# Kernel tuning notes

Hardware: AMD Instinct MI355X
Metric: run time of the kernel (lower is better)

## Reference

```python
import jax, jax.numpy as jnp
import numpy as np

RTOL = 1e-3
ATOL = 1e-3
MAX_STEPS = 16   # static bound on adaptive dopri5 iterations (accepted+rejected)
H0 = 0.05        # initial step size (torchdiffeq picks this heuristically)


def _mlp(t1, y, z, w1, b1, w2, b2, t_eval):
    # TimeRescale: t = t1 * t_eval; dH/dt1 = hazard(t, y, z) * t_eval
    tt = t1 * t_eval                                   # [B,1]
    x = jnp.concatenate([tt, y, z], axis=1)            # [B, latent+2]
    h = jax.nn.relu(x @ w1.T + b1)                     # [B, 2*(latent+2)]
    return jax.nn.softplus(h @ w2.T + b2) * t_eval     # [B,1]


def _dopri5(f, y0, t1=1.0):
    """Adaptive Dormand-Prince RK45 from t=0 to t=t1 with a static step budget."""
    f0 = f(jnp.float32(0.0), y0)

    def body(i, carry):
        t, y, fy, h, done = carry
        h = jnp.minimum(h, t1 - t)
        k1 = fy
        k2 = f(t + 0.2 * h, y + h * (0.2 * k1))
        k3 = f(t + 0.3 * h, y + h * (3/40 * k1 + 9/40 * k2))
        k4 = f(t + 0.8 * h, y + h * (44/45 * k1 - 56/15 * k2 + 32/9 * k3))
        k5 = f(t + 8/9 * h, y + h * (19372/6561 * k1 - 25360/2187 * k2 + 64448/6561 * k3 - 212/729 * k4))
        k6 = f(t + h, y + h * (9017/3168 * k1 - 355/33 * k2 + 46732/5247 * k3 + 49/176 * k4 - 5103/18656 * k5))
        y5 = y + h * (35/384 * k1 + 500/1113 * k3 + 125/192 * k4 - 2187/6784 * k5 + 11/84 * k6)
        k7 = f(t + h, y5)  # FSAL
        err = h * (71/57600 * k1 - 71/16695 * k3 + 71/1920 * k4 - 17253/339200 * k5 + 22/525 * k6 - 1/40 * k7)
        scale = ATOL + RTOL * jnp.maximum(jnp.abs(y), jnp.abs(y5))
        en = jnp.sqrt(jnp.mean((err / scale) ** 2))
        accept = (en <= 1.0) & (~done)
        fac = jnp.clip(0.9 * jnp.power(jnp.maximum(en, 1e-10), -0.2), 0.2, 10.0)
        t_n = jnp.where(accept, t + h, t)
        y_n = jnp.where(accept, y5, y)
        f_n = jnp.where(accept, k7, fy)
        h_n = jnp.where(done, h, h * fac)
        done_n = done | (t_n >= t1 - 1e-9)
        return (t_n, y_n, f_n, h_n, done_n)

    carry = (jnp.float32(0.0), y0, f0, jnp.float32(H0), jnp.array(False))
    _, yT, _, _, _ = jax.lax.fori_loop(0, MAX_STEPS, body, carry)
    return yT


def setup_inputs() -> dict:
    key = jax.random.key(0)
    ks = jax.random.split(key, 6)
    B, D, R = 4096, 128, 2
    IN, HID = D + 2, 2 * (D + 2)
    s = 1.0 / np.sqrt(IN)
    return {
        "z": jax.random.normal(ks[0], (B, D), jnp.float32),
        "t_eval": jax.random.uniform(ks[1], (B, 1), jnp.float32, 0.1, 3.0),
        "w1": jax.random.normal(ks[2], (R, HID, IN), jnp.float32) * s,
        "b1": jax.random.normal(ks[3], (R, HID), jnp.float32) * s,
        "w2": jax.random.normal(ks[4], (R, 1, HID), jnp.float32) * (1.0 / np.sqrt(HID)),
        "b2": jax.random.normal(ks[5], (R, 1), jnp.float32) * 0.01,
    }


def reference(z, t_eval, w1, b1, w2, b2):
    B = z.shape[0]
    R = w1.shape[0]
    y0 = jnp.zeros((B, 1), z.dtype)
    t_rec = jnp.where(t_eval != 0, 1.0 / t_eval, 0.0)
    haz_list, chf_list = [], []
    for r in range(R):
        f = lambda t, y, r=r: _mlp(t, y, z, w1[r], b1[r], w2[r], b2[r], t_eval)
        yT = _dopri5(f, y0)                       # CHF at rescaled t=1
        haz = t_rec * f(jnp.float32(1.0), yT)     # [B,1]
        chf = jnp.stack([y0, yT], axis=0)          # [2,B,1] (t_points = [0,1])
        chf_list.append(jnp.transpose(chf, (1, 0, 2)))  # [B,2,1]
        haz_list.append(haz.T)                           # [1,B]
    return (jnp.stack(haz_list, axis=0), jnp.stack(chf_list, axis=0))  # [R,1,B], [R,B,2,1]
```

## Files before the change

### kernel.cpp

```cpp
#include <hip/hip_runtime.h>
#include <math.h>


#define B_ 4096
#define R_ 2
#define D_ 128
#define IN_ 130
#define HID_ 260
#define NU_ 17
#define JP_ 272
#define KP_ 136

#define WS_P_      0
#define WS_ACW_    (R_ * B_ * JP_)

typedef __attribute__((ext_vector_type(8))) short  short8;
typedef __attribute__((ext_vector_type(4))) float  floatx4;

__device__ __forceinline__ unsigned short f2bf_rn(float x) {
    unsigned int u = __float_as_uint(x);
    unsigned int r = (u + 0x7FFFu + ((u >> 16) & 1u)) >> 16;
    return (unsigned short)r;
}
__device__ __forceinline__ float bf2f(unsigned short h) {
    return __uint_as_float(((unsigned int)h) << 16);
}

__global__ __launch_bounds__(256) void k1_gemm(
    const float* __restrict__ z, const float* __restrict__ w1,
    const float* __restrict__ b1, const float* __restrict__ w2,
    float* __restrict__ ws)
{
    __shared__ unsigned short sWh[64 * KP_];
    __shared__ unsigned short sWl[64 * KP_];
    __shared__ unsigned short sZh[64 * KP_];
    __shared__ unsigned short sZl[64 * KP_];

    const int t  = threadIdx.x;
    const int r  = blockIdx.x / 320;
    const int jt = (blockIdx.x % 320) >> 6;
    const int bt = blockIdx.x & 63;
    const int j0 = jt * 64;
    const int b0 = bt * 64;

    const float* w1r = w1 + r * HID_ * IN_;

    if (bt == 0 && t < 64) {
        const int j = j0 + t;
        if (j < HID_) {
            const float2 ac = *(const float2*)(w1r + j * IN_);
            float* acw = ws + WS_ACW_ + r * 3 * JP_;
            acw[0 * JP_ + j] = ac.x;
            acw[1 * JP_ + j] = ac.y;
            acw[2 * JP_ + j] = w2[r * HID_ + j];
        }
    }

    {
        const int row = t >> 2;
        const int ks  = (t & 3) * 32;
        const float* src = z + (b0 + row) * D_ + ks;
        unsigned short* dh = sZh + row * KP_ + ks;
        unsigned short* dl = sZl + row * KP_ + ks;
#pragma unroll
        for (int q = 0; q < 8; ++q) {
            const float4 v = *(const float4*)(src + q * 4);
            short4 hq, lq;
            {
                const unsigned short h0 = f2bf_rn(v.x); const float p0 = v.x - bf2f(h0);
                const unsigned short h1 = f2bf_rn(v.y); const float p1 = v.y - bf2f(h1);
                const unsigned short h2 = f2bf_rn(v.z); const float p2 = v.z - bf2f(h2);
                const unsigned short h3 = f2bf_rn(v.w); const float p3 = v.w - bf2f(h3);
                hq = make_short4((short)h0, (short)h1, (short)h2, (short)h3);
                lq = make_short4((short)f2bf_rn(p0), (short)f2bf_rn(p1),
                                 (short)f2bf_rn(p2), (short)f2bf_rn(p3));
            }
            *(short4*)(dh + q * 4) = hq;
            *(short4*)(dl + q * 4) = lq;
        }
    }

    {
        const int row = t >> 2;
        const int ks  = (t & 3) * 32;
        const int j   = j0 + row;
        unsigned short* dh = sWh + row * KP_ + ks;
        unsigned short* dl = sWl + row * KP_ + ks;
        if (j < HID_) {
            const float* src = w1r + j * IN_ + 2 + ks;
#pragma unroll
            for (int q = 0; q < 16; ++q) {
                const float2 v = *(const float2*)(src + q * 2);
                const unsigned short h0 = f2bf_rn(v.x); const float p0 = v.x - bf2f(h0);
                const unsigned short h1 = f2bf_rn(v.y); const float p1 = v.y - bf2f(h1);
                *(short2*)(dh + q * 2) = make_short2((short)h0, (short)h1);
                *(short2*)(dl + q * 2) = make_short2((short)f2bf_rn(p0), (short)f2bf_rn(p1));
            }
        } else {
            const short4 zz = make_short4(0, 0, 0, 0);
#pragma unroll
            for (int q = 0; q < 8; ++q) {
                *(short4*)(dh + q * 4) = zz;
                *(short4*)(dl + q * 4) = zz;
            }
        }
    }
    __syncthreads();

    const int wv   = t >> 6;
    const int lane = t & 63;
    const int lm   = lane & 15;
    const int quad = lane >> 4;

    short8 Ah[4], Al[4];
    {
        const unsigned short* aph = sWh + (wv * 16 + lm) * KP_ + quad * 8;
        const unsigned short* apl = sWl + (wv * 16 + lm) * KP_ + quad * 8;
#pragma unroll
        for (int ks = 0; ks < 4; ++ks) {
            Ah[ks] = *(const short8*)(aph + ks * 32);
            Al[ks] = *(const short8*)(apl + ks * 32);
        }
    }

    const int jrow = j0 + wv * 16 + quad * 4;
    float bj0 = 0.f, bj1 = 0.f, bj2 = 0.f, bj3 = 0.f;
    if (jrow < HID_) {
        const float* bb = b1 + r * HID_ + jrow;
        bj0 = bb[0]; bj1 = bb[1]; bj2 = bb[2]; bj3 = bb[3];
    }

#pragma unroll
    for (int bs = 0; bs < 4; ++bs) {
        floatx4 acc = {0.f, 0.f, 0.f, 0.f};
        const unsigned short* bph = sZh + (bs * 16 + lm) * KP_ + quad * 8;
        const unsigned short* bpl = sZl + (bs * 16 + lm) * KP_ + quad * 8;
#pragma unroll
        for (int ks = 0; ks < 4; ++ks) {
            const short8 Bh = *(const short8*)(bph + ks * 32);
            const short8 Bl = *(const short8*)(bpl + ks * 32);
            acc = __builtin_amdgcn_mfma_f32_16x16x32_bf16(Ah[ks], Bh, acc, 0, 0, 0);
            acc = __builtin_amdgcn_mfma_f32_16x16x32_bf16(Ah[ks], Bl, acc, 0, 0, 0);
            acc = __builtin_amdgcn_mfma_f32_16x16x32_bf16(Al[ks], Bh, acc, 0, 0, 0);
        }
        if (jrow < HID_) {
            const int b = b0 + bs * 16 + lm;
            float4 o;
            o.x = acc[0] + bj0;
            o.y = acc[1] + bj1;
            o.z = acc[2] + bj2;
            o.w = acc[3] + bj3;
            *(float4*)(ws + WS_P_ + (r * B_ + b) * JP_ + jrow) = o;
        }
    }
}

__device__ __forceinline__ float dpp_add16(float v) {
    int y;
    y = __builtin_amdgcn_update_dpp(0, __float_as_int(v), 0xB1, 0xF, 0xF, false);
    v += __int_as_float(y);
    y = __builtin_amdgcn_update_dpp(0, __float_as_int(v), 0x4E, 0xF, 0xF, false);
    v += __int_as_float(y);
    y = __builtin_amdgcn_update_dpp(0, __float_as_int(v), 0x124, 0xF, 0xF, false);
    v += __int_as_float(y);
    y = __builtin_amdgcn_update_dpp(0, __float_as_int(v), 0x128, 0xF, 0xF, false);
    v += __int_as_float(y);
    return v;
}

__device__ __forceinline__ float softplus_fast(float x) {
    const float q  = exp2f(-1.4426950408889634f * fabsf(x));
    const float lg = 0.6931471805599453f * log2f(1.0f + q);
    return fmaxf(x, 0.0f) + lg;
}

__global__ __launch_bounds__(256) void k2_solve(
    const float* __restrict__ t_eval, const float* __restrict__ b2,
    const float* __restrict__ ws, float* __restrict__ out)
{
    const int sub = threadIdx.x & 15;
    const int T   = blockIdx.x * 16 + (threadIdx.x >> 4);
    const int r   = T >> 12;
    const int b   = T & (B_ - 1);

    const float te = t_eval[b];

    float P[NU_], A[NU_], C[NU_], W[NU_];
    const float* pp  = ws + WS_P_ + (r * B_ + b) * JP_;
    const float* acw = ws + WS_ACW_ + r * 3 * JP_;
#pragma unroll
    for (int i = 0; i < NU_; ++i) {
        const int j = sub + (i << 4);
        if (j < HID_) {
            P[i] = pp[j];
            A[i] = acw[0 * JP_ + j];
            C[i] = acw[1 * JP_ + j];
            W[i] = acw[2 * JP_ + j];
        } else {
            P[i] = A[i] = C[i] = W[i] = 0.f;
        }
    }
    const float b2r = b2[r];

    auto feval = [&](float t1, float yv) -> float {
        const float tt = t1 * te;
        float d0 = 0.f, d1 = 0.f;
#pragma unroll
        for (int i = 0; i < NU_; ++i) {
            const float hv = fmaf(tt, A[i], fmaf(yv, C[i], P[i]));
            if (i & 1) d1 = fmaf(W[i], fmaxf(hv, 0.f), d1);
            else       d0 = fmaf(W[i], fmaxf(hv, 0.f), d0);
        }
        const float dot = dpp_add16(d0 + d1);
        return softplus_fast(dot + b2r) * te;
    };

    const float h  = 0.125f;
    const float hh = 0.0625f;
    float y = 0.f;
#pragma unroll 1
    for (int s = 0; s < 8; ++s) {
        const float t0 = (float)s * h;
        const float k1 = feval(t0,      y);
        const float k2 = feval(t0 + hh, fmaf(hh, k1, y));
        const float k3 = feval(t0 + hh, fmaf(hh, k2, y));
        const float k4 = feval(t0 + h,  fmaf(h,  k3, y));
        y = fmaf(h * (1.f / 6.f), k1 + 2.f * (k2 + k3) + k4, y);
    }

    const float yT = y;
    const float hazf = feval(1.0f, yT);
    const float t_rec = (te != 0.f) ? (1.f / te) : 0.f;

    if (sub == 0) {
        out[r * B_ + b] = t_rec * hazf;
        const int base = R_ * B_ + (r * B_ + b) * 2;
        out[base + 0] = 0.f;
        out[base + 1] = yT;
    }
}

extern "C" void kernel_launch(void* const* d_in, const int* in_sizes, int n_in,
                              void* d_out, int out_size, void* d_ws, size_t ws_size,
                              hipStream_t stream) {
    const float* z      = (const float*)d_in[0];
    const float* t_eval = (const float*)d_in[1];
    const float* w1     = (const float*)d_in[2];
    const float* b1     = (const float*)d_in[3];
    const float* w2     = (const float*)d_in[4];
    const float* b2     = (const float*)d_in[5];
    float* out = (float*)d_out;
    float* ws  = (float*)d_ws;

    hipLaunchKernelGGL(k1_gemm, dim3(640), dim3(256), 0, stream,
                       z, w1, b1, w2, ws);
    hipLaunchKernelGGL(k2_solve, dim3(512), dim3(256), 0, stream,
                       t_eval, b2, ws, out);
}
```

Before: 86.80 us.

## Fuse GEMM prologue and ODE solve into one kernel using shared memory

Merges the bf16-split MFMA projection kernel and the per-row dopri5 solve kernel into a single kernel. Each block computes the hidden pre-activations for its 16 rows directly into LDS, removing the global workspace round trip and the second launch. In exchange every block re-reads and re-converts the full w1 matrix for its head, and the larger LDS footprint may reduce occupancy during the solve phase.

```diff
diff --git a/kernel.cpp b/kernel.cpp
--- a/kernel.cpp
+++ b/kernel.cpp
@@ -8,11 +8,8 @@
 #define IN_ 130
 #define HID_ 260
 #define NU_ 17
-#define JP_ 272
 #define KP_ 136
-
-#define WS_P_      0
-#define WS_ACW_    (R_ * B_ * JP_)
+#define PP_ 272
 
 typedef __attribute__((ext_vector_type(8))) short  short8;
 typedef __attribute__((ext_vector_type(4))) float  floatx4;
@@ -26,135 +23,6 @@
     return __uint_as_float(((unsigned int)h) << 16);
 }
 
-__global__ __launch_bounds__(256) void k1_gemm(
-    const float* __restrict__ z, const float* __restrict__ w1,
-    const float* __restrict__ b1, const float* __restrict__ w2,
-    float* __restrict__ ws)
-{
-    __shared__ unsigned short sWh[64 * KP_];
-    __shared__ unsigned short sWl[64 * KP_];
-    __shared__ unsigned short sZh[64 * KP_];
-    __shared__ unsigned short sZl[64 * KP_];
-
-    const int t  = threadIdx.x;
-    const int r  = blockIdx.x / 320;
-    const int jt = (blockIdx.x % 320) >> 6;
-    const int bt = blockIdx.x & 63;
-    const int j0 = jt * 64;
-    const int b0 = bt * 64;
-
-    const float* w1r = w1 + r * HID_ * IN_;
-
-    if (bt == 0 && t < 64) {
-        const int j = j0 + t;
-        if (j < HID_) {
-            const float2 ac = *(const float2*)(w1r + j * IN_);
-            float* acw = ws + WS_ACW_ + r * 3 * JP_;
-            acw[0 * JP_ + j] = ac.x;
-            acw[1 * JP_ + j] = ac.y;
-            acw[2 * JP_ + j] = w2[r * HID_ + j];
-        }
-    }
-
-    {
-        const int row = t >> 2;
-        const int ks  = (t & 3) * 32;
-        const float* src = z + (b0 + row) * D_ + ks;
-        unsigned short* dh = sZh + row * KP_ + ks;
-        unsigned short* dl = sZl + row * KP_ + ks;
-#pragma unroll
-        for (int q = 0; q < 8; ++q) {
-            const float4 v = *(const float4*)(src + q * 4);
-            short4 hq, lq;
-            {
-                const unsigned short h0 = f2bf_rn(v.x); const float p0 = v.x - bf2f(h0);
-                const unsigned short h1 = f2bf_rn(v.y); const float p1 = v.y - bf2f(h1);
-                const unsigned short h2 = f2bf_rn(v.z); const float p2 = v.z - bf2f(h2);
-                const unsigned short h3 = f2bf_rn(v.w); const float p3 = v.w - bf2f(h3);
-                hq = make_short4((short)h0, (short)h1, (short)h2, (short)h3);
-                lq = make_short4((short)f2bf_rn(p0), (short)f2bf_rn(p1),
-                                 (short)f2bf_rn(p2), (short)f2bf_rn(p3));
-            }
-            *(short4*)(dh + q * 4) = hq;
-            *(short4*)(dl + q * 4) = lq;
-        }
-    }
-
-    {
-        const int row = t >> 2;
-        const int ks  = (t & 3) * 32;
-        const int j   = j0 + row;
-        unsigned short* dh = sWh + row * KP_ + ks;
-        unsigned short* dl = sWl + row * KP_ + ks;
-        if (j < HID_) {
-            const float* src = w1r + j * IN_ + 2 + ks;
-#pragma unroll
-            for (int q = 0; q < 16; ++q) {
-                const float2 v = *(const float2*)(src + q * 2);
-                const unsigned short h0 = f2bf_rn(v.x); const float p0 = v.x - bf2f(h0);
-                const unsigned short h1 = f2bf_rn(v.y); const float p1 = v.y - bf2f(h1);
-                *(short2*)(dh + q * 2) = make_short2((short)h0, (short)h1);
-                *(short2*)(dl + q * 2) = make_short2((short)f2bf_rn(p0), (short)f2bf_rn(p1));
-            }
-        } else {
-            const short4 zz = make_short4(0, 0, 0, 0);
-#pragma unroll
-            for (int q = 0; q < 8; ++q) {
-                *(short4*)(dh + q * 4) = zz;
-                *(short4*)(dl + q * 4) = zz;
-            }
-        }
-    }
-    __syncthreads();
-
-    const int wv   = t >> 6;
-    const int lane = t & 63;
-    const int lm   = lane & 15;
-    const int quad = lane >> 4;
-
-    short8 Ah[4], Al[4];
-    {
-        const unsigned short* aph = sWh + (wv * 16 + lm) * KP_ + quad * 8;
-        const unsigned short* apl = sWl + (wv * 16 + lm) * KP_ + quad * 8;
-#pragma unroll
-        for (int ks = 0; ks < 4; ++ks) {
-            Ah[ks] = *(const short8*)(aph + ks * 32);
-            Al[ks] = *(const short8*)(apl + ks * 32);
-        }
-    }
-
-    const int jrow = j0 + wv * 16 + quad * 4;
-    float bj0 = 0.f, bj1 = 0.f, bj2 = 0.f, bj3 = 0.f;
-    if (jrow < HID_) {
-        const float* bb = b1 + r * HID_ + jrow;
-        bj0 = bb[0]; bj1 = bb[1]; bj2 = bb[2]; bj3 = bb[3];
-    }
-
-#pragma unroll
-    for (int bs = 0; bs < 4; ++bs) {
-        floatx4 acc = {0.f, 0.f, 0.f, 0.f};
-        const unsigned short* bph = sZh + (bs * 16 + lm) * KP_ + quad * 8;
-        const unsigned short* bpl = sZl + (bs * 16 + lm) * KP_ + quad * 8;
-#pragma unroll
-        for (int ks = 0; ks < 4; ++ks) {
-            const short8 Bh = *(const short8*)(bph + ks * 32);
-            const short8 Bl = *(const short8*)(bpl + ks * 32);
-            acc = __builtin_amdgcn_mfma_f32_16x16x32_bf16(Ah[ks], Bh, acc, 0, 0, 0);
-            acc = __builtin_amdgcn_mfma_f32_16x16x32_bf16(Ah[ks], Bl, acc, 0, 0, 0);
-            acc = __builtin_amdgcn_mfma_f32_16x16x32_bf16(Al[ks], Bh, acc, 0, 0, 0);
-        }
-        if (jrow < HID_) {
-            const int b = b0 + bs * 16 + lm;
-            float4 o;
-            o.x = acc[0] + bj0;
-            o.y = acc[1] + bj1;
-            o.z = acc[2] + bj2;
-            o.w = acc[3] + bj3;
-            *(float4*)(ws + WS_P_ + (r * B_ + b) * JP_ + jrow) = o;
-        }
-    }
-}
-
 __device__ __forceinline__ float dpp_add16(float v) {
     int y;
     y = __builtin_amdgcn_update_dpp(0, __float_as_int(v), 0xB1, 0xF, 0xF, false);
@@ -174,31 +42,127 @@
     return fmaxf(x, 0.0f) + lg;
 }
 
-__global__ __launch_bounds__(256) void k2_solve(
-    const float* __restrict__ t_eval, const float* __restrict__ b2,
-    const float* __restrict__ ws, float* __restrict__ out)
+__global__ __launch_bounds__(256) void cr_fused(
+    const float* __restrict__ z, const float* __restrict__ t_eval,
+    const float* __restrict__ w1, const float* __restrict__ b1,
+    const float* __restrict__ w2, const float* __restrict__ b2,
+    float* __restrict__ out)
 {
-    const int sub = threadIdx.x & 15;
-    const int T   = blockIdx.x * 16 + (threadIdx.x >> 4);
-    const int r   = T >> 12;
-    const int b   = T & (B_ - 1);
-
+    __shared__ unsigned short sWh[64 * KP_];
+    __shared__ unsigned short sWl[64 * KP_];
+    __shared__ unsigned short sZh[16 * KP_];
+    __shared__ unsigned short sZl[16 * KP_];
+    __shared__ float sP[16 * PP_];
+    __shared__ float sA[PP_], sC[PP_], sWo[PP_], sB1[PP_];
+
+    const int t   = threadIdx.x;
+    const int r   = blockIdx.x >> 8;
+    const int b0  = (blockIdx.x & 255) * 16;
+    const float* w1r = w1 + r * HID_ * IN_;
+
+    for (int j = t; j < PP_; j += 256) {
+        float av = 0.f, cv = 0.f, wv = 0.f, bv = 0.f;
+        if (j < HID_) {
+            const float2 ac = *(const float2*)(w1r + j * IN_);
+            av = ac.x; cv = ac.y;
+            wv = w2[r * HID_ + j];
+            bv = b1[r * HID_ + j];
+        }
+        sA[j] = av; sC[j] = cv; sWo[j] = wv; sB1[j] = bv;
+    }
+
+    {
+        const int row = t >> 4;
+        const int c0  = (t & 15) * 8;
+        const float* src = z + (b0 + row) * D_ + c0;
+        unsigned short* dh = sZh + row * KP_ + c0;
+        unsigned short* dl = sZl + row * KP_ + c0;
+#pragma unroll
+        for (int q = 0; q < 2; ++q) {
+            const float4 v = *(const float4*)(src + q * 4);
+            const unsigned short h0 = f2bf_rn(v.x); const float p0 = v.x - bf2f(h0);
+            const unsigned short h1 = f2bf_rn(v.y); const float p1 = v.y - bf2f(h1);
+            const unsigned short h2 = f2bf_rn(v.z); const float p2 = v.z - bf2f(h2);
+            const unsigned short h3 = f2bf_rn(v.w); const float p3 = v.w - bf2f(h3);
+            *(short4*)(dh + q * 4) = make_short4((short)h0, (short)h1, (short)h2, (short)h3);
+            *(short4*)(dl + q * 4) = make_short4((short)f2bf_rn(p0), (short)f2bf_rn(p1),
+                                                 (short)f2bf_rn(p2), (short)f2bf_rn(p3));
+        }
+    }
+
+    const int wv_  = t >> 6;
+    const int lane = t & 63;
+    const int lm   = lane & 15;
+    const int quad = lane >> 4;
+
+    for (int c = 0; c < 5; ++c) {
+        const int j0c = c * 64;
+        if (c > 0) __syncthreads();
+        {
+            const int row = t >> 2;
+            const int ks  = (t & 3) * 32;
+            const int j   = j0c + row;
+            unsigned short* dh = sWh + row * KP_ + ks;
+            unsigned short* dl = sWl + row * KP_ + ks;
+            if (j < HID_) {
+                const float* src = w1r + j * IN_ + 2 + ks;
+#pragma unroll
+                for (int q = 0; q < 16; ++q) {
+                    const float2 v = *(const float2*)(src + q * 2);
+                    const unsigned short h0 = f2bf_rn(v.x); const float p0 = v.x - bf2f(h0);
+                    const unsigned short h1 = f2bf_rn(v.y); const float p1 = v.y - bf2f(h1);
+                    *(short2*)(dh + q * 2) = make_short2((short)h0, (short)h1);
+                    *(short2*)(dl + q * 2) = make_short2((short)f2bf_rn(p0), (short)f2bf_rn(p1));
+                }
+            } else {
+                const short4 zz = make_short4(0, 0, 0, 0);
+#pragma unroll
+                for (int q = 0; q < 8; ++q) {
+                    *(short4*)(dh + q * 4) = zz;
+                    *(short4*)(dl + q * 4) = zz;
+                }
+            }
+        }
+        __syncthreads();
+
+        floatx4 acc = {0.f, 0.f, 0.f, 0.f};
+        const unsigned short* aph = sWh + (wv_ * 16 + lm) * KP_ + quad * 8;
+        const unsigned short* apl = sWl + (wv_ * 16 + lm) * KP_ + quad * 8;
+        const unsigned short* bph = sZh + lm * KP_ + quad * 8;
+        const unsigned short* bpl = sZl + lm * KP_ + quad * 8;
+#pragma unroll
+        for (int ks = 0; ks < 4; ++ks) {
+            const short8 Ah = *(const short8*)(aph + ks * 32);
+            const short8 Al = *(const short8*)(apl + ks * 32);
+            const short8 Bh = *(const short8*)(bph + ks * 32);
+            const short8 Bl = *(const short8*)(bpl + ks * 32);
+            acc = __builtin_amdgcn_mfma_f32_16x16x32_bf16(Ah, Bh, acc, 0, 0, 0);
+            acc = __builtin_amdgcn_mfma_f32_16x16x32_bf16(Ah, Bl, acc, 0, 0, 0);
+            acc = __builtin_amdgcn_mfma_f32_16x16x32_bf16(Al, Bh, acc, 0, 0, 0);
+        }
+        const int jrow = j0c + wv_ * 16 + quad * 4;
+        if (jrow < PP_) {
+            float4 o;
+            o.x = acc[0]; o.y = acc[1]; o.z = acc[2]; o.w = acc[3];
+            *(float4*)(sP + lm * PP_ + jrow) = o;
+        }
+    }
+    __syncthreads();
+
+    const int sub = t & 15;
+    const int g   = t >> 4;
+    const int b   = b0 + g;
     const float te = t_eval[b];
 
     float P[NU_], A[NU_], C[NU_], W[NU_];
-    const float* pp  = ws + WS_P_ + (r * B_ + b) * JP_;
-    const float* acw = ws + WS_ACW_ + r * 3 * JP_;
+    const float* pg = sP + g * PP_;
 #pragma unroll
     for (int i = 0; i < NU_; ++i) {
         const int j = sub + (i << 4);
-        if (j < HID_) {
-            P[i] = pp[j];
-            A[i] = acw[0 * JP_ + j];
-            C[i] = acw[1 * JP_ + j];
-            W[i] = acw[2 * JP_ + j];
-        } else {
-            P[i] = A[i] = C[i] = W[i] = 0.f;
-        }
+        P[i] = pg[j] + sB1[j];
+        A[i] = sA[j];
+        C[i] = sC[j];
+        W[i] = sWo[j];
     }
     const float b2r = b2[r];
 
@@ -250,10 +214,7 @@
     const float* w2     = (const float*)d_in[4];
     const float* b2     = (const float*)d_in[5];
     float* out = (float*)d_out;
-    float* ws  = (float*)d_ws;
-
-    hipLaunchKernelGGL(k1_gemm, dim3(640), dim3(256), 0, stream,
-                       z, w1, b1, w2, ws);
-    hipLaunchKernelGGL(k2_solve, dim3(512), dim3(256), 0, stream,
-                       t_eval, b2, ws, out);
-}
+
+    hipLaunchKernelGGL(cr_fused, dim3(512), dim3(256), 0, stream,
+                       z, t_eval, w1, b1, w2, b2, out);
+}
```

Measured after the change: 85.58 us. Within noise of the previous version (-1.4%).
